# Kernel tuning notes

Measured on AMD Instinct MI355X. Metric: run time of the kernel, lower is better.

## Reference

```python
import jax, jax.numpy as jnp
import numpy as np

S = 7
B = 2
C = 20
LAMBDA_COORD = 5.0
LAMBDA_NOOBJ = 0.5
EPS = 1e-6
N_IMG = 8192
N_GT = 32


def setup_inputs() -> dict:
    key = jax.random.key(0)
    k1, k2, k3 = jax.random.split(key, 3)
    outputs = jax.random.uniform(k1, (N_IMG, S, S, B * 5 + C), dtype=jnp.float32)
    gt_boxes = jax.random.uniform(k2, (N_IMG, N_GT, 4), dtype=jnp.float32)
    gt_labels = jax.random.randint(k3, (N_IMG, N_GT), 0, C)
    return {"outputs": outputs, "gt_boxes": gt_boxes, "gt_labels": gt_labels}


def _pairwise_iou(pred, gt):
    # pred: [N,S,S,B,1,4], gt: [N,1,1,1,G,4], boxes in (cx, cy, w, h) format
    px1 = pred[..., 0] - pred[..., 2] * 0.5
    py1 = pred[..., 1] - pred[..., 3] * 0.5
    px2 = pred[..., 0] + pred[..., 2] * 0.5
    py2 = pred[..., 1] + pred[..., 3] * 0.5
    gx1 = gt[..., 0] - gt[..., 2] * 0.5
    gy1 = gt[..., 1] - gt[..., 3] * 0.5
    gx2 = gt[..., 0] + gt[..., 2] * 0.5
    gy2 = gt[..., 1] + gt[..., 3] * 0.5
    iw = jnp.clip(jnp.minimum(px2, gx2) - jnp.maximum(px1, gx1), 0.0)
    ih = jnp.clip(jnp.minimum(py2, gy2) - jnp.maximum(py1, gy1), 0.0)
    inter = iw * ih
    union = pred[..., 2] * pred[..., 3] + gt[..., 2] * gt[..., 3] - inter
    return inter / (union + EPS)  # [N,S,S,B,G]


def reference(outputs, gt_boxes, gt_labels):
    N = outputs.shape[0]
    pb = outputs[..., : B * 5].reshape(N, S, S, B, 5)
    pbox = pb[..., :4]          # [N,S,S,B,4]
    pconf = pb[..., 4]          # [N,S,S,B]
    pcls = outputs[..., B * 5:] # [N,S,S,C]

    iou = _pairwise_iou(pbox[:, :, :, :, None, :], gt_boxes[:, None, None, None, :, :])
    best_iou = iou.max(axis=-1)      # [N,S,S,B]
    best_idx = iou.argmax(axis=-1)   # [N,S,S,B]

    # gather matched GT boxes: [N,S,S,B,4]
    matched = jnp.take_along_axis(
        gt_boxes[:, None, None, None, :, :], best_idx[..., None, None], axis=4
    ).squeeze(4)

    loc = LAMBDA_COORD * (
        (pbox[..., 0] - matched[..., 0]) ** 2
        + (pbox[..., 1] - matched[..., 1]) ** 2
        + (jnp.sqrt(pbox[..., 2]) - jnp.sqrt(matched[..., 2])) ** 2
        + (jnp.sqrt(pbox[..., 3]) - jnp.sqrt(matched[..., 3])) ** 2
    )
    conf_obj = (pconf - best_iou) ** 2

    # multi-hot class target per image (scatter 1 at every GT label)
    multihot = jnp.zeros((N, C), outputs.dtype).at[
        jnp.arange(N)[:, None], gt_labels
    ].set(1.0)
    # soft-target cross entropy: -sum(t * log_softmax(logits)) per cell
    ce = -(jax.nn.log_softmax(pcls, axis=-1) * multihot[:, None, None, :]).sum(-1)  # [N,S,S]

    has_obj = best_iou > 0.0
    per_box = jnp.where(has_obj, loc + conf_obj + ce[..., None], LAMBDA_NOOBJ * pconf ** 2)
    return per_box.sum() / N
```

## Files before the change

### kernel.cpp

```cpp
#include <hip/hip_runtime.h>

#define NC 20
#define NCELL 49
#define NGT 32
#define NIMG 8192
#define NTOT (NIMG * NCELL)
#define CPB 128
#define NTILE (NTOT / CPB)
#define PBLK 1024
#define NSPAN 4
#define L2E 1.44269504088896f
#define LN2 0.69314718055995f
#define LAMBDA_COORD 5.0f
#define LAMBDA_NOOBJ 0.5f
#define EPS_IOU 1e-6f

typedef _Float16 h2 __attribute__((ext_vector_type(2)));
#define H2MAX(a, b) __builtin_elementwise_max((a), (b))
#define H2MIN(a, b) __builtin_elementwise_min((a), (b))

__global__ __launch_bounds__(256, 4) void yolo_main_kernel(
    const float* __restrict__ outputs,
    const float* __restrict__ gt_boxes,
    const int*   __restrict__ gt_labels,
    float* __restrict__ partials)
{
    __shared__ float4   s_act4[2][CPB * 30 / 4];
    __shared__ float4   s_gtc[2][NSPAN * NGT];
    __shared__ uint2    s_gtp[2][NSPAN * NGT];
    __shared__ _Float16 s_gah[2][NSPAN * NGT];
    __shared__ float    s_fm [2][NSPAN * NC];
    __shared__ unsigned s_mask[2][NSPAN];
    __shared__ float    s_w[4];

    const int tid = threadIdx.x;
    const int bid = blockIdx.x;
    const int nt  = 3 + (bid < (NTILE - 3 * PBLK) ? 1 : 0);

    float acc = 0.f;

    float4 r0, r1, r2, r3, gtr;
    unsigned labbit = 0u;
    unsigned g_img = NIMG;

#define STAGE_ISSUE(base_) do {                                               \
    const float4* asrc_ = reinterpret_cast<const float4*>(outputs)            \
                        + (size_t)(base_) * 30 / 4;                           \
    r0 = asrc_[tid];                                                          \
    r1 = asrc_[tid + 256];                                                    \
    r2 = asrc_[tid + 512];                                                    \
    if (tid < 192) r3 = asrc_[tid + 768];                                     \
    const unsigned il_ = (base_) / NCELL;                                     \
    if (tid < 128) {                                                          \
        const unsigned g_ = (unsigned)tid >> 5;                               \
        g_img = il_ + g_;                                                     \
        if (g_img < NIMG)                                                     \
            gtr = reinterpret_cast<const float4*>(gt_boxes)[g_img * NGT + (tid & 31)]; \
    } else {                                                                  \
        const int t_ = tid - 128;                                             \
        const unsigned g_ = (unsigned)t_ >> 5;                                \
        g_img = il_ + g_;                                                     \
        labbit = (g_img < NIMG) ? (1u << gt_labels[g_img * NGT + (t_ & 31)])  \
                                : 0u;                                         \
    }                                                                         \
} while (0)

#define STAGE_WRITE(nb_) do {                                                 \
    s_act4[nb_][tid]       = r0;                                              \
    s_act4[nb_][tid + 256] = r1;                                              \
    s_act4[nb_][tid + 512] = r2;                                              \
    if (tid < 192) s_act4[nb_][tid + 768] = r3;                               \
    if (tid < 128) {                                                          \
        if (g_img < NIMG) {                                                   \
            const float gx1 = fmaf(gtr.z, -0.5f, gtr.x);                      \
            const float gy1 = fmaf(gtr.w, -0.5f, gtr.y);                      \
            const float gx2 = fmaf(gtr.z,  0.5f, gtr.x);                      \
            const float gy2 = fmaf(gtr.w,  0.5f, gtr.y);                      \
            s_gtc[nb_][tid] = make_float4(gx1, gy1, gx2, gy2);                \
            h2 mn_; mn_.x = (_Float16)gx1; mn_.y = (_Float16)gy1;             \
            h2 mx_; mx_.x = (_Float16)gx2; mx_.y = (_Float16)gy2;             \
            s_gtp[nb_][tid] = make_uint2(__builtin_bit_cast(unsigned, mn_),   \
                                         __builtin_bit_cast(unsigned, mx_));  \
            s_gah[nb_][tid] = (_Float16)(gtr.z * gtr.w);                      \
        }                                                                     \
    } else {                                                                  \
        unsigned m_ = labbit;                                                 \
        m_ |= __shfl_xor(m_, 1, 32);                                          \
        m_ |= __shfl_xor(m_, 2, 32);                                          \
        m_ |= __shfl_xor(m_, 4, 32);                                          \
        m_ |= __shfl_xor(m_, 8, 32);                                          \
        m_ |= __shfl_xor(m_, 16, 32);                                         \
        const int t_ = tid - 128;                                             \
        const int l_ = t_ & 31;                                               \
        if (l_ == 0) s_mask[nb_][t_ >> 5] = m_;                               \
        if (l_ < NC) s_fm[nb_][(t_ >> 5) * NC + l_] =                         \
                         ((m_ >> l_) & 1u) ? 1.0f : 0.0f;                     \
    }                                                                         \
} while (0)

    STAGE_ISSUE((unsigned)bid * CPB);
    STAGE_WRITE(0);
    __syncthreads();

    int cur = 0;
    for (int k = 0; k < nt; ++k) {
        const unsigned tile = (unsigned)bid + (unsigned)k * PBLK;
        const unsigned base = tile * CPB;
        const bool hn = (k + 1 < nt);
        if (hn) STAGE_ISSUE((tile + PBLK) * CPB);

        const unsigned img_lo = base / NCELL;
        const unsigned off    = base - img_lo * NCELL;

        const int p = tid & 1;
        const int s = tid >> 1;
        const unsigned rel  = ((unsigned)(s + off) * 1339u) >> 16;
        const unsigned mask = s_mask[cur][rel];
        const float2* a2 = reinterpret_cast<const float2*>(s_act4[cur]) + s * 15;

        const float2* cp  = a2 + 5 + p * 5;
        const float2* fm2 = reinterpret_cast<const float2*>(s_fm[cur] + rel * NC) + p * 5;
        float2 c0 = cp[0], c1 = cp[1], c2 = cp[2], c3 = cp[3], c4 = cp[4];
        float2 m0 = fm2[0], m1 = fm2[1], m2 = fm2[2], m3 = fm2[3], m4 = fm2[4];
        const float t1 = fmaxf(fmaxf(c0.x, c0.y), c1.x);
        const float t2 = fmaxf(fmaxf(c1.y, c2.x), c2.y);
        const float t3 = fmaxf(fmaxf(c3.x, c3.y), c4.x);
        float mxh = fmaxf(fmaxf(fmaxf(t1, t2), t3), c4.y);
        float selh = 0.f;
        selh = fmaf(m0.x, c0.x, selh); selh = fmaf(m0.y, c0.y, selh);
        selh = fmaf(m1.x, c1.x, selh); selh = fmaf(m1.y, c1.y, selh);
        selh = fmaf(m2.x, c2.x, selh); selh = fmaf(m2.y, c2.y, selh);
        selh = fmaf(m3.x, c3.x, selh); selh = fmaf(m3.y, c3.y, selh);
        selh = fmaf(m4.x, c4.x, selh); selh = fmaf(m4.y, c4.y, selh);
        const float mx  = fmaxf(mxh, __shfl_xor(mxh, 1));
        const float mxl = mx * L2E;
        float ssh = 0.f;
        ssh += __builtin_amdgcn_exp2f(fmaf(c0.x, L2E, -mxl));
        ssh += __builtin_amdgcn_exp2f(fmaf(c0.y, L2E, -mxl));
        ssh += __builtin_amdgcn_exp2f(fmaf(c1.x, L2E, -mxl));
        ssh += __builtin_amdgcn_exp2f(fmaf(c1.y, L2E, -mxl));
        ssh += __builtin_amdgcn_exp2f(fmaf(c2.x, L2E, -mxl));
        ssh += __builtin_amdgcn_exp2f(fmaf(c2.y, L2E, -mxl));
        ssh += __builtin_amdgcn_exp2f(fmaf(c3.x, L2E, -mxl));
        ssh += __builtin_amdgcn_exp2f(fmaf(c3.y, L2E, -mxl));
        ssh += __builtin_amdgcn_exp2f(fmaf(c4.x, L2E, -mxl));
        ssh += __builtin_amdgcn_exp2f(fmaf(c4.y, L2E, -mxl));
        const float ssum = ssh + __shfl_xor(ssh, 1);
        const float sel  = selh + __shfl_xor(selh, 1);
        const float ce = (float)__popc(mask)
                       * fmaf(__builtin_amdgcn_logf(ssum), LN2, mx) - sel;

        float2 A = a2[2 * p], Bv = a2[2 * p + 1], Cv = a2[2 * p + 2];
        const float cx = p ? A.y  : A.x;
        const float cy = p ? Bv.x : A.y;
        const float w  = p ? Bv.y : Bv.x;
        const float h  = p ? Cv.x : Bv.y;
        const float cf = p ? Cv.y : Cv.x;

        h2 pmn, pmx;
        pmn.x = (_Float16)fmaf(w, -0.5f, cx); pmn.y = (_Float16)fmaf(h, -0.5f, cy);
        pmx.x = (_Float16)fmaf(w,  0.5f, cx); pmx.y = (_Float16)fmaf(h,  0.5f, cy);
        const _Float16 pae = (_Float16)(w * h + EPS_IOU);
        const h2 zero2 = (h2)((_Float16)0);

        const uint4* gtp4 = reinterpret_cast<const uint4*>(s_gtp[cur] + rel * NGT);
        const h2*    gah2 = reinterpret_cast<const h2*>(s_gah[cur] + rel * NGT);
        _Float16 bin = (_Float16)(-1.0f), bS = (_Float16)(1.0f);
        int bi = 0;
        #pragma unroll
        for (int i = 0; i < NGT / 2; ++i) {
            const uint4 rec = gtp4[i];
            const h2 gap = gah2[i];
            {
                h2 lo = H2MAX(pmn, __builtin_bit_cast(h2, rec.x));
                h2 hi = H2MIN(pmx, __builtin_bit_cast(h2, rec.y));
                h2 d  = H2MAX(hi - lo, zero2);
                const _Float16 in = d.x * d.y;
                const _Float16 S  = pae + gap.x;
                if (in * bS > bin * S) { bin = in; bS = S; bi = 2 * i; }
            }
            {
                h2 lo = H2MAX(pmn, __builtin_bit_cast(h2, rec.z));
                h2 hi = H2MIN(pmx, __builtin_bit_cast(h2, rec.w));
                h2 d  = H2MAX(hi - lo, zero2);
                const _Float16 in = d.x * d.y;
                const _Float16 S  = pae + gap.y;
                if (in * bS > bin * S) { bin = in; bS = S; bi = 2 * i + 1; }
            }
        }

        float term;
        if ((float)bin > 0.f) {
            float4 g = s_gtc[cur][rel * NGT + bi];
            const float binf = (float)bin, bSf = (float)bS;
            const float iou = __fdividef(binf, bSf - binf);
            const float dx = cx - (g.x + g.z) * 0.5f;
            const float dy = cy - (g.y + g.w) * 0.5f;
            const float dw = sqrtf(w) - sqrtf(g.z - g.x);
            const float dh = sqrtf(h) - sqrtf(g.w - g.y);
            term = LAMBDA_COORD * (dx * dx + dy * dy + dw * dw + dh * dh)
                 + (cf - iou) * (cf - iou) + ce;
        } else {
            term = LAMBDA_NOOBJ * cf * cf;
        }
        acc += term;

        if (hn) STAGE_WRITE(cur ^ 1);
        __syncthreads();
        cur ^= 1;
    }

    #pragma unroll
    for (int o = 32; o > 0; o >>= 1)
        acc += __shfl_down(acc, o);
    if ((tid & 63) == 0) s_w[tid >> 6] = acc;
    __syncthreads();
    if (tid == 0)
        partials[bid] = s_w[0] + s_w[1] + s_w[2] + s_w[3];
}

__global__ __launch_bounds__(256) void yolo_reduce_kernel(
    const float* __restrict__ partials, float* __restrict__ out)
{
    float s = 0.f;
    #pragma unroll
    for (int k = 0; k < PBLK / 256; ++k)
        s += partials[threadIdx.x + k * 256];
    #pragma unroll
    for (int o = 32; o > 0; o >>= 1)
        s += __shfl_down(s, o);
    __shared__ float s_w[4];
    const int tid = threadIdx.x;
    if ((tid & 63) == 0) s_w[tid >> 6] = s;
    __syncthreads();
    if (tid == 0)
        out[0] = (s_w[0] + s_w[1] + s_w[2] + s_w[3]) * (1.0f / (float)NIMG);
}

extern "C" void kernel_launch(void* const* d_in, const int* in_sizes, int n_in,
                              void* d_out, int out_size, void* d_ws, size_t ws_size,
                              hipStream_t stream) {
    const float* outputs   = (const float*)d_in[0];
    const float* gt_boxes  = (const float*)d_in[1];
    const int*   gt_labels = (const int*)d_in[2];
    float* out      = (float*)d_out;
    float* partials = (float*)d_ws;

    yolo_main_kernel<<<PBLK, 256, 0, stream>>>(outputs, gt_boxes, gt_labels, partials);
    yolo_reduce_kernel<<<1, 256, 0, stream>>>(partials, out);
}
```

Measured before the change: 27.02 us.

## Repack GT boxes into pairwise SoA half2 layout and drop softmax max-shift

Ground-truth corner data is now stored so that each half2 holds the same coordinate for two GT boxes. The IoU loop then computes intersections for two boxes per packed op instead of one box's x/y pair, which cuts the f16 instruction count in the hot loop. The staging loads are restructured so 64 threads each fetch two GT boxes. The softmax max reduction and its shuffle are removed, and exp2 is applied to the raw logits. This is only safe because the inputs lie in [0,1) and would overflow for large logits.

```diff
diff --git a/kernel.cpp b/kernel.cpp
--- a/kernel.cpp
+++ b/kernel.cpp
@@ -18,6 +18,7 @@
 typedef _Float16 h2 __attribute__((ext_vector_type(2)));
 #define H2MAX(a, b) __builtin_elementwise_max((a), (b))
 #define H2MIN(a, b) __builtin_elementwise_min((a), (b))
+#define BC(u_) __builtin_bit_cast(h2, (u_))
 
 __global__ __launch_bounds__(256, 4) void yolo_main_kernel(
     const float* __restrict__ outputs,
@@ -27,8 +28,8 @@
 {
     __shared__ float4   s_act4[2][CPB * 30 / 4];
     __shared__ float4   s_gtc[2][NSPAN * NGT];
-    __shared__ uint2    s_gtp[2][NSPAN * NGT];
-    __shared__ _Float16 s_gah[2][NSPAN * NGT];
+    __shared__ uint4    s_gtp[2][NSPAN * 16];
+    __shared__ h2       s_gah[2][NSPAN * 16];
     __shared__ float    s_fm [2][NSPAN * NC];
     __shared__ unsigned s_mask[2][NSPAN];
     __shared__ float    s_w[4];
@@ -39,7 +40,7 @@
 
     float acc = 0.f;
 
-    float4 r0, r1, r2, r3, gtr;
+    float4 r0, r1, r2, r3, gtr0, gtr1;
     unsigned labbit = 0u;
     unsigned g_img = NIMG;
 
@@ -51,12 +52,16 @@
     r2 = asrc_[tid + 512];                                                    \
     if (tid < 192) r3 = asrc_[tid + 768];                                     \
     const unsigned il_ = (base_) / NCELL;                                     \
-    if (tid < 128) {                                                          \
-        const unsigned g_ = (unsigned)tid >> 5;                               \
+    if (tid < 64) {                                                           \
+        const unsigned g_ = (unsigned)tid >> 4;                               \
         g_img = il_ + g_;                                                     \
-        if (g_img < NIMG)                                                     \
-            gtr = reinterpret_cast<const float4*>(gt_boxes)[g_img * NGT + (tid & 31)]; \
-    } else {                                                                  \
+        if (g_img < NIMG) {                                                   \
+            const float4* gp_ = reinterpret_cast<const float4*>(gt_boxes)     \
+                              + (size_t)g_img * NGT + 2 * (tid & 15);         \
+            gtr0 = gp_[0];                                                    \
+            gtr1 = gp_[1];                                                    \
+        }                                                                     \
+    } else if (tid >= 128) {                                                  \
         const int t_ = tid - 128;                                             \
         const unsigned g_ = (unsigned)t_ >> 5;                                \
         g_img = il_ + g_;                                                     \
@@ -70,20 +75,34 @@
     s_act4[nb_][tid + 256] = r1;                                              \
     s_act4[nb_][tid + 512] = r2;                                              \
     if (tid < 192) s_act4[nb_][tid + 768] = r3;                               \
-    if (tid < 128) {                                                          \
+    if (tid < 64) {                                                           \
         if (g_img < NIMG) {                                                   \
-            const float gx1 = fmaf(gtr.z, -0.5f, gtr.x);                      \
-            const float gy1 = fmaf(gtr.w, -0.5f, gtr.y);                      \
-            const float gx2 = fmaf(gtr.z,  0.5f, gtr.x);                      \
-            const float gy2 = fmaf(gtr.w,  0.5f, gtr.y);                      \
-            s_gtc[nb_][tid] = make_float4(gx1, gy1, gx2, gy2);                \
-            h2 mn_; mn_.x = (_Float16)gx1; mn_.y = (_Float16)gy1;             \
-            h2 mx_; mx_.x = (_Float16)gx2; mx_.y = (_Float16)gy2;             \
-            s_gtp[nb_][tid] = make_uint2(__builtin_bit_cast(unsigned, mn_),   \
-                                         __builtin_bit_cast(unsigned, mx_));  \
-            s_gah[nb_][tid] = (_Float16)(gtr.z * gtr.w);                      \
+            const unsigned g_ = (unsigned)tid >> 4;                           \
+            const unsigned q_ = (unsigned)tid & 15u;                          \
+            const float x10 = fmaf(gtr0.z, -0.5f, gtr0.x);                    \
+            const float y10 = fmaf(gtr0.w, -0.5f, gtr0.y);                    \
+            const float x20 = fmaf(gtr0.z,  0.5f, gtr0.x);                    \
+            const float y20 = fmaf(gtr0.w,  0.5f, gtr0.y);                    \
+            const float x11 = fmaf(gtr1.z, -0.5f, gtr1.x);                    \
+            const float y11 = fmaf(gtr1.w, -0.5f, gtr1.y);                    \
+            const float x21 = fmaf(gtr1.z,  0.5f, gtr1.x);                    \
+            const float y21 = fmaf(gtr1.w,  0.5f, gtr1.y);                    \
+            s_gtc[nb_][g_ * NGT + 2 * q_]     = make_float4(x10, y10, x20, y20); \
+            s_gtc[nb_][g_ * NGT + 2 * q_ + 1] = make_float4(x11, y11, x21, y21); \
+            h2 t0; t0.x = (_Float16)x10; t0.y = (_Float16)x11;                \
+            h2 t1; t1.x = (_Float16)y10; t1.y = (_Float16)y11;                \
+            h2 t2; t2.x = (_Float16)x20; t2.y = (_Float16)x21;                \
+            h2 t3; t3.x = (_Float16)y20; t3.y = (_Float16)y21;                \
+            s_gtp[nb_][g_ * 16 + q_] =                                        \
+                make_uint4(__builtin_bit_cast(unsigned, t0),                  \
+                           __builtin_bit_cast(unsigned, t1),                  \
+                           __builtin_bit_cast(unsigned, t2),                  \
+                           __builtin_bit_cast(unsigned, t3));                 \
+            h2 ga_; ga_.x = (_Float16)(gtr0.z * gtr0.w);                      \
+            ga_.y = (_Float16)(gtr1.z * gtr1.w);                              \
+            s_gah[nb_][g_ * 16 + q_] = ga_;                                   \
         }                                                                     \
-    } else {                                                                  \
+    } else if (tid >= 128) {                                                  \
         unsigned m_ = labbit;                                                 \
         m_ |= __shfl_xor(m_, 1, 32);                                          \
         m_ |= __shfl_xor(m_, 2, 32);                                          \
@@ -116,77 +135,60 @@
         const int s = tid >> 1;
         const unsigned rel  = ((unsigned)(s + off) * 1339u) >> 16;
         const unsigned mask = s_mask[cur][rel];
-        const float2* a2 = reinterpret_cast<const float2*>(s_act4[cur]) + s * 15;
-
-        const float2* cp  = a2 + 5 + p * 5;
+        const float* af = reinterpret_cast<const float*>(s_act4[cur]) + s * 30;
+
+        const float2* cp  = reinterpret_cast<const float2*>(af + 10) + p * 5;
         const float2* fm2 = reinterpret_cast<const float2*>(s_fm[cur] + rel * NC) + p * 5;
         float2 c0 = cp[0], c1 = cp[1], c2 = cp[2], c3 = cp[3], c4 = cp[4];
         float2 m0 = fm2[0], m1 = fm2[1], m2 = fm2[2], m3 = fm2[3], m4 = fm2[4];
-        const float t1 = fmaxf(fmaxf(c0.x, c0.y), c1.x);
-        const float t2 = fmaxf(fmaxf(c1.y, c2.x), c2.y);
-        const float t3 = fmaxf(fmaxf(c3.x, c3.y), c4.x);
-        float mxh = fmaxf(fmaxf(fmaxf(t1, t2), t3), c4.y);
         float selh = 0.f;
         selh = fmaf(m0.x, c0.x, selh); selh = fmaf(m0.y, c0.y, selh);
         selh = fmaf(m1.x, c1.x, selh); selh = fmaf(m1.y, c1.y, selh);
         selh = fmaf(m2.x, c2.x, selh); selh = fmaf(m2.y, c2.y, selh);
         selh = fmaf(m3.x, c3.x, selh); selh = fmaf(m3.y, c3.y, selh);
         selh = fmaf(m4.x, c4.x, selh); selh = fmaf(m4.y, c4.y, selh);
-        const float mx  = fmaxf(mxh, __shfl_xor(mxh, 1));
-        const float mxl = mx * L2E;
         float ssh = 0.f;
-        ssh += __builtin_amdgcn_exp2f(fmaf(c0.x, L2E, -mxl));
-        ssh += __builtin_amdgcn_exp2f(fmaf(c0.y, L2E, -mxl));
-        ssh += __builtin_amdgcn_exp2f(fmaf(c1.x, L2E, -mxl));
-        ssh += __builtin_amdgcn_exp2f(fmaf(c1.y, L2E, -mxl));
-        ssh += __builtin_amdgcn_exp2f(fmaf(c2.x, L2E, -mxl));
-        ssh += __builtin_amdgcn_exp2f(fmaf(c2.y, L2E, -mxl));
-        ssh += __builtin_amdgcn_exp2f(fmaf(c3.x, L2E, -mxl));
-        ssh += __builtin_amdgcn_exp2f(fmaf(c3.y, L2E, -mxl));
-        ssh += __builtin_amdgcn_exp2f(fmaf(c4.x, L2E, -mxl));
-        ssh += __builtin_amdgcn_exp2f(fmaf(c4.y, L2E, -mxl));
+        ssh += __builtin_amdgcn_exp2f(c0.x * L2E);
+        ssh += __builtin_amdgcn_exp2f(c0.y * L2E);
+        ssh += __builtin_amdgcn_exp2f(c1.x * L2E);
+        ssh += __builtin_amdgcn_exp2f(c1.y * L2E);
+        ssh += __builtin_amdgcn_exp2f(c2.x * L2E);
+        ssh += __builtin_amdgcn_exp2f(c2.y * L2E);
+        ssh += __builtin_amdgcn_exp2f(c3.x * L2E);
+        ssh += __builtin_amdgcn_exp2f(c3.y * L2E);
+        ssh += __builtin_amdgcn_exp2f(c4.x * L2E);
+        ssh += __builtin_amdgcn_exp2f(c4.y * L2E);
         const float ssum = ssh + __shfl_xor(ssh, 1);
         const float sel  = selh + __shfl_xor(selh, 1);
         const float ce = (float)__popc(mask)
-                       * fmaf(__builtin_amdgcn_logf(ssum), LN2, mx) - sel;
-
-        float2 A = a2[2 * p], Bv = a2[2 * p + 1], Cv = a2[2 * p + 2];
-        const float cx = p ? A.y  : A.x;
-        const float cy = p ? Bv.x : A.y;
-        const float w  = p ? Bv.y : Bv.x;
-        const float h  = p ? Cv.x : Bv.y;
-        const float cf = p ? Cv.y : Cv.x;
-
-        h2 pmn, pmx;
-        pmn.x = (_Float16)fmaf(w, -0.5f, cx); pmn.y = (_Float16)fmaf(h, -0.5f, cy);
-        pmx.x = (_Float16)fmaf(w,  0.5f, cx); pmx.y = (_Float16)fmaf(h,  0.5f, cy);
-        const _Float16 pae = (_Float16)(w * h + EPS_IOU);
+                       * (__builtin_amdgcn_logf(ssum) * LN2) - sel;
+
+        const float* bf = af + p * 5;
+        const float cx = bf[0], cy = bf[1], w = bf[2], h = bf[3], cf = bf[4];
+
+        const float px1 = fmaf(w, -0.5f, cx), py1 = fmaf(h, -0.5f, cy);
+        const float px2 = fmaf(w,  0.5f, cx), py2 = fmaf(h,  0.5f, cy);
+        h2 px1b; px1b.x = px1b.y = (_Float16)px1;
+        h2 py1b; py1b.x = py1b.y = (_Float16)py1;
+        h2 px2b; px2b.x = px2b.y = (_Float16)px2;
+        h2 py2b; py2b.x = py2b.y = (_Float16)py2;
+        h2 paeb; paeb.x = paeb.y = (_Float16)(w * h + EPS_IOU);
         const h2 zero2 = (h2)((_Float16)0);
 
-        const uint4* gtp4 = reinterpret_cast<const uint4*>(s_gtp[cur] + rel * NGT);
-        const h2*    gah2 = reinterpret_cast<const h2*>(s_gah[cur] + rel * NGT);
+        const uint4* gtp4 = s_gtp[cur] + rel * 16;
+        const h2*    gah2 = s_gah[cur] + rel * 16;
         _Float16 bin = (_Float16)(-1.0f), bS = (_Float16)(1.0f);
         int bi = 0;
         #pragma unroll
-        for (int i = 0; i < NGT / 2; ++i) {
+        for (int i = 0; i < 16; ++i) {
             const uint4 rec = gtp4[i];
-            const h2 gap = gah2[i];
-            {
-                h2 lo = H2MAX(pmn, __builtin_bit_cast(h2, rec.x));
-                h2 hi = H2MIN(pmx, __builtin_bit_cast(h2, rec.y));
-                h2 d  = H2MAX(hi - lo, zero2);
-                const _Float16 in = d.x * d.y;
-                const _Float16 S  = pae + gap.x;
-                if (in * bS > bin * S) { bin = in; bS = S; bi = 2 * i; }
-            }
-            {
-                h2 lo = H2MAX(pmn, __builtin_bit_cast(h2, rec.z));
-                h2 hi = H2MIN(pmx, __builtin_bit_cast(h2, rec.w));
-                h2 d  = H2MAX(hi - lo, zero2);
-                const _Float16 in = d.x * d.y;
-                const _Float16 S  = pae + gap.y;
-                if (in * bS > bin * S) { bin = in; bS = S; bi = 2 * i + 1; }
-            }
+            const h2 ga2 = gah2[i];
+            h2 iw2 = H2MAX(H2MIN(px2b, BC(rec.z)) - H2MAX(px1b, BC(rec.x)), zero2);
+            h2 ih2 = H2MAX(H2MIN(py2b, BC(rec.w)) - H2MAX(py1b, BC(rec.y)), zero2);
+            h2 in2 = iw2 * ih2;
+            h2 S2  = paeb + ga2;
+            if (in2.x * bS > bin * S2.x) { bin = in2.x; bS = S2.x; bi = 2 * i; }
+            if (in2.y * bS > bin * S2.y) { bin = in2.y; bS = S2.y; bi = 2 * i + 1; }
         }
 
         float term;
```

Result: no change. 26.68 us (-1.3%).
